# Optimization experiments

Hardware: AMD Instinct MI355X
Metric: run time of the kernel (lower is better)

Reference implementation:

```python
import jax, jax.numpy as jnp
import numpy as np

N = 50000          # nodes
E = 800000         # edges (avg degree 16)
NODE_IN, NODE_OUT = 64, 96
EDGE_IN, EDGE_OUT = 32, 32
CONV = [192, 192]  # hidden_conv_sizes
LIN = [192]        # hidden_linear_sizes
NUM_CLASSES = 2


def _linear_init(k, fan_in, fan_out):
    s = 1.0 / np.sqrt(fan_in)
    kw, kb = jax.random.split(k)
    W = jax.random.uniform(kw, (fan_in, fan_out), jnp.float32, -s, s)
    b = jax.random.uniform(kb, (fan_out,), jnp.float32, -s, s)
    return W, b


def setup_inputs() -> dict:
    key = jax.random.key(0)
    ks = jax.random.split(key, 10)
    node_feats = jax.random.normal(ks[0], (N, NODE_IN), jnp.float32)
    edge_feats = jax.random.normal(ks[1], (E, EDGE_IN), jnp.float32)
    src = jax.random.randint(ks[2], (E,), 0, N)
    dst = jax.random.randint(ks[3], (E,), 0, N)
    Wn, bn = _linear_init(ks[4], NODE_IN, NODE_OUT)
    We, be = _linear_init(ks[5], EDGE_IN, EDGE_OUT)
    Wc0, bc0 = _linear_init(ks[6], NODE_OUT + EDGE_OUT, CONV[0])
    Wc1, bc1 = _linear_init(ks[7], CONV[0], CONV[1])
    Wl0, bl0 = _linear_init(ks[8], CONV[1], LIN[0])
    Wo, bo = _linear_init(ks[9], LIN[0], NUM_CLASSES)
    return dict(node_feats=node_feats, edge_feats=edge_feats,
                Wn=Wn, bn=bn, We=We, be=be,
                Wc0=Wc0, bc0=bc0, Wc1=Wc1, bc1=bc1,
                Wl0=Wl0, bl0=bl0, Wo=Wo, bo=bo,
                src=src, dst=dst)


def reference(node_feats, edge_feats, Wn, bn, We, be, Wc0, bc0, Wc1, bc1,
              Wl0, bl0, Wo, bo, src, dst):
    ones = jnp.ones((E,), jnp.float32)
    deg_in = jnp.clip(jax.ops.segment_sum(ones, dst, num_segments=N), 1.0)
    deg_out = jnp.clip(jax.ops.segment_sum(ones, src, num_segments=N), 1.0)
    inv_in = jax.lax.rsqrt(deg_in)    # D_in^{-1/2}
    inv_out = jax.lax.rsqrt(deg_out)  # D_out^{-1/2}

    # EdgeLayer: per-edge linear, mean-aggregated onto destination nodes
    eh = edge_feats @ We + be                                   # [E, EDGE_OUT]
    edge_h = jax.nn.relu(
        jax.ops.segment_sum(eh, dst, num_segments=N) / deg_in[:, None])

    # NodeEmbeddingLayer: per-node linear
    node_h = jax.nn.relu(node_feats @ Wn + bn)                  # [N, NODE_OUT]

    h = jnp.concatenate([edge_h, node_h], axis=1)               # [N, EDGE_OUT+NODE_OUT]

    # dgl GraphConv (norm='both'): D_in^{-1/2} A D_out^{-1/2} h W + b
    # dropout is identity in eval mode
    for W, b in ((Wc0, bc0), (Wc1, bc1)):
        msg = (h * inv_out[:, None])[src]                       # [E, d] gather
        agg = jax.ops.segment_sum(msg, dst, num_segments=N) * inv_in[:, None]
        h = jax.nn.relu(agg @ W + b)

    h = jax.nn.relu(h @ Wl0 + bl0)
    return h @ Wo + bo                                          # [N, NUM_CLASSES]
```

## Files before the change

kernel.cpp:

```cpp
#include <hip/hip_runtime.h>

#define NN 50000
#define NE 800000
#define CAP 64

#define NPB 128
#define NBKT 391
#define NBKT_PAD 512
#define BCAP 3072
#define CHUNK 4096

typedef unsigned short u16;
typedef unsigned int u32;
typedef unsigned long long u64;
typedef __attribute__((ext_vector_type(8))) short bf8_t;
typedef __attribute__((ext_vector_type(4))) float f4_t;

__device__ __forceinline__ u16 f2b(float f) {
    unsigned u = __float_as_uint(f);
    unsigned r = u + 0x7FFF + ((u >> 16) & 1);
    return (u16)(r >> 16);
}

__global__ __launch_bounds__(256) void partition_k(
    const int* __restrict__ src, const int* __restrict__ dst,
    int* __restrict__ deg_out, int* __restrict__ bktc,
    u64* __restrict__ part, int E) {
    __shared__ unsigned cnt[NBKT_PAD];
    __shared__ unsigned base[NBKT_PAD];
    __shared__ unsigned cur[NBKT_PAD];
    __shared__ unsigned gbase[NBKT_PAD];
    __shared__ unsigned wtot[4];
    __shared__ u64 staged[CHUNK];

    const int tid = threadIdx.x;
    const int lane = tid & 63;
    const int wid = tid >> 6;
    const int e0 = blockIdx.x * CHUNK;
    const int n = min(CHUNK, E - e0);

    for (int i = tid; i < NBKT_PAD; i += 256) cnt[i] = 0;
    __syncthreads();

    for (int i = tid; i < n; i += 256) {
        int d = dst[e0 + i];
        atomicAdd(&cnt[d >> 7], 1u);
    }
    __syncthreads();

    {
        unsigned a = cnt[2 * tid];
        unsigned b = cnt[2 * tid + 1];
        unsigned ps = a + b;
        unsigned inc = ps;
#pragma unroll
        for (int d = 1; d < 64; d <<= 1) {
            unsigned v = __shfl_up(inc, d);
            if (lane >= d) inc += v;
        }
        if (lane == 63) wtot[wid] = inc;
        __syncthreads();
        unsigned wb = 0;
#pragma unroll
        for (int k = 0; k < 4; ++k) wb += (k < wid) ? wtot[k] : 0;
        unsigned eb = wb + inc - ps;
        base[2 * tid] = eb;
        base[2 * tid + 1] = eb + a;
        cur[2 * tid] = eb;
        cur[2 * tid + 1] = eb + a;
    }
    __syncthreads();

    for (int i = tid; i < n; i += 256) {
        int e = e0 + i;
        int d = dst[e];
        int s = src[e];
        atomicAdd(deg_out + s, 1);
        unsigned p = atomicAdd(&cur[d >> 7], 1u);
        staged[p] = ((u64)(unsigned)e << 32) | (((u32)d << 16) | (u32)s);
    }
    __syncthreads();

    for (int b = tid; b < NBKT; b += 256) {
        unsigned c = cur[b] - base[b];
        if (c) gbase[b] = (unsigned)atomicAdd(&bktc[b], (int)c);
    }
    __syncthreads();

    for (int i = tid; i < n; i += 256) {
        u64 v = staged[i];
        int b = (int)((v >> 16) & 0xffffu) >> 7;
        unsigned idx = gbase[b] + ((unsigned)i - base[b]);
        if (idx < BCAP) part[(size_t)b * BCAP + idx] = v;
    }
}

__global__ __launch_bounds__(256) void fill_k(
    const u64* __restrict__ part, const int* __restrict__ bktc,
    int* __restrict__ csr_src, int* __restrict__ csr_eid,
    int* __restrict__ din, int n) {
    __shared__ unsigned cur[NPB];
    const int tid = threadIdx.x;
    const int b = blockIdx.x;
    const int node0 = b << 7;
    if (tid < NPB) cur[tid] = 0;
    __syncthreads();

    const int cnt = min(bktc[b], BCAP);
    const u64* p = part + (size_t)b * BCAP;
    for (int i = tid; i < cnt; i += 256) {
        u64 v = p[i];
        int s = (int)(v & 0xffffu);
        int d = (int)((v >> 16) & 0xffffu);
        int e = (int)(v >> 32);
        unsigned q = atomicAdd(&cur[d & (NPB - 1)], 1u);
        if (q < CAP) {
            csr_src[((size_t)d << 6) + q] = s;
            csr_eid[((size_t)d << 6) + q] = e;
        }
    }
    __syncthreads();
    if (tid < NPB) {
        int node = node0 + tid;
        if (node < n) {
            unsigned cq = min(cur[tid], (unsigned)CAP);
            din[node] = (int)cq;
            int end = (cq <= 32u) ? 32 : 64;
            for (int q = (int)cq; q < end; ++q)
                csr_eid[((size_t)node << 6) + q] = 0;
        }
    }
}

__global__ void make_inv_k(const int* __restrict__ deg_in, const int* __restrict__ deg_out,
                           float* __restrict__ inv_in, float* __restrict__ inv_out,
                           float* __restrict__ inv_mean, float* __restrict__ bcoef, int n) {
    int i = blockIdx.x * 256 + threadIdx.x;
    if (i < n) {
        int d_in = deg_in[i];
        float di = fmaxf((float)d_in, 1.0f);
        float dq = fmaxf((float)deg_out[i], 1.0f);
        inv_in[i]   = 1.0f / sqrtf(di);
        inv_out[i]  = 1.0f / sqrtf(dq);
        inv_mean[i] = 1.0f / di;
        bcoef[i]    = (d_in > 0) ? 1.0f : 0.0f;
    }
}

__global__ __launch_bounds__(256) void gather_e4_k(
    const float* __restrict__ ef, const int* __restrict__ csr_eid,
    const int* __restrict__ deg, float* __restrict__ efa) {
    const int lane = threadIdx.x & 63;
    const int node = __builtin_amdgcn_readfirstlane(blockIdx.x * 4 + (threadIdx.x >> 6));
    const int beg = node << 6;
    const int cnt = deg[node];
    const int g = lane >> 4;
    const int c = (lane & 15) * 2;

    float ax = 0.0f, ay = 0.0f;
    {
        int eidv[8];
#pragma unroll
        for (int j = 0; j < 8; ++j) eidv[j] = csr_eid[beg + 4 * j + g];
        float2 v[8];
#pragma unroll
        for (int j = 0; j < 8; ++j)
            v[j] = *(const float2*)(ef + (size_t)eidv[j] * 32 + c);
#pragma unroll
        for (int j = 0; j < 8; ++j)
            if (4 * j + g < cnt) { ax += v[j].x; ay += v[j].y; }
    }
    if (cnt > 32) {
        int eidv[8];
#pragma unroll
        for (int j = 0; j < 8; ++j) eidv[j] = csr_eid[beg + 32 + 4 * j + g];
        float2 v[8];
#pragma unroll
        for (int j = 0; j < 8; ++j)
            v[j] = *(const float2*)(ef + (size_t)eidv[j] * 32 + c);
#pragma unroll
        for (int j = 0; j < 8; ++j)
            if (32 + 4 * j + g < cnt) { ax += v[j].x; ay += v[j].y; }
    }
    ax += __shfl_down(ax, 16); ay += __shfl_down(ay, 16);
    ax += __shfl_down(ax, 32); ay += __shfl_down(ay, 32);
    if (lane < 16) {
        float2 o; o.x = ax; o.y = ay;
        *(float2*)(efa + (size_t)node * 32 + c) = o;
    }
}

template <int D, int LPT>
__global__ __launch_bounds__(256) void gather_b2_k(
    const u16* __restrict__ h, const int* __restrict__ csr,
    const int* __restrict__ deg, const float* __restrict__ inv_in,
    u16* __restrict__ agg) {
    constexpr int ACT = D / LPT;
    constexpr int NW = LPT / 2;
    const int lane = threadIdx.x & 63;
    const int node = __builtin_amdgcn_readfirstlane(blockIdx.x * 4 + (threadIdx.x >> 6));
    const int beg = node << 6;
    const int cnt = deg[node];
    const int off = (lane < ACT ? lane : ACT - 1) * LPT;

    float acc[LPT];
#pragma unroll
    for (int j = 0; j < LPT; ++j) acc[j] = 0.0f;

    const int nb = cnt >> 4;
    int idx[16];
    if (nb > 0) {
#pragma unroll
        for (int j = 0; j < 16; ++j) idx[j] = csr[beg + j];
    }
    for (int b = 0; b < nb; ++b) {
        unsigned lv[16][NW];
#pragma unroll
        for (int j = 0; j < 16; ++j) {
            const unsigned* p = (const unsigned*)(h + (size_t)idx[j] * D + off);
            if constexpr (NW == 2) {
                uint2 t = *(const uint2*)p;
                lv[j][0] = t.x; lv[j][1] = t.y;
            } else {
                lv[j][0] = *p;
            }
        }
        int nidx[16];
        const int nbase = beg + (b + 1) * 16;
        if (b + 1 < nb) {
#pragma unroll
            for (int j = 0; j < 16; ++j) nidx[j] = csr[nbase + j];
        }
#pragma unroll
        for (int j = 0; j < 16; ++j)
#pragma unroll
            for (int q = 0; q < NW; ++q) {
                unsigned u = lv[j][q];
                acc[2 * q]     += __uint_as_float(u << 16);
                acc[2 * q + 1] += __uint_as_float(u & 0xffff0000u);
            }
        if (b + 1 < nb) {
#pragma unroll
            for (int j = 0; j < 16; ++j) idx[j] = nidx[j];
        }
    }

    int tb = beg + (nb << 4);
    int rem = cnt & 15;
    if (rem >= 8) {
        int ti[8];
#pragma unroll
        for (int j = 0; j < 8; ++j) ti[j] = csr[tb + j];
        unsigned lv[8][NW];
#pragma unroll
        for (int j = 0; j < 8; ++j) {
            const unsigned* p = (const unsigned*)(h + (size_t)ti[j] * D + off);
            if constexpr (NW == 2) {
                uint2 t = *(const uint2*)p;
                lv[j][0] = t.x; lv[j][1] = t.y;
            } else {
                lv[j][0] = *p;
            }
        }
#pragma unroll
        for (int j = 0; j < 8; ++j)
#pragma unroll
            for (int q = 0; q < NW; ++q) {
                unsigned u = lv[j][q];
                acc[2 * q]     += __uint_as_float(u << 16);
                acc[2 * q + 1] += __uint_as_float(u & 0xffff0000u);
            }
        tb += 8;
        rem -= 8;
    }
    for (int t = 0; t < rem; ++t) {
        const unsigned* p = (const unsigned*)(h + (size_t)csr[tb + t] * D + off);
#pragma unroll
        for (int q = 0; q < NW; ++q) {
            unsigned u = p[q];
            acc[2 * q]     += __uint_as_float(u << 16);
            acc[2 * q + 1] += __uint_as_float(u & 0xffff0000u);
        }
    }

    if (lane < ACT) {
        float sc = inv_in[node];
        unsigned o[NW];
#pragma unroll
        for (int q = 0; q < NW; ++q)
            o[q] = (unsigned)f2b(acc[2 * q] * sc) | ((unsigned)f2b(acc[2 * q + 1] * sc) << 16);
        unsigned* dp = (unsigned*)(agg + (size_t)node * D + off);
        if constexpr (NW == 2) {
            uint2 t; t.x = o[0]; t.y = o[1];
            *(uint2*)dp = t;
        } else {
            *dp = o[0];
        }
    }
}

template <int D_IN, int D_OUT, bool SCALE, bool BROW>
__global__ __launch_bounds__(256) void gemm_tile_k(
    const float* __restrict__ in, int in_stride,
    const float* __restrict__ W, const float* __restrict__ bias,
    const float* __restrict__ scale, const float* __restrict__ brow,
    const float* __restrict__ posts,
    u16* __restrict__ out, int out_stride, int n) {
    constexpr int TMW = 8;
    constexpr int ROWS = TMW * 4;
    constexpr int NOUT = (D_OUT + 63) / 64;
    __shared__ float s_in[ROWS * D_IN];

    const int tid = threadIdx.x;
    const int lane = tid & 63;
    const int wave = tid >> 6;
    const int row0 = blockIdx.x * ROWS;

    constexpr int NV = ROWS * D_IN / 4;
    for (int i = tid; i < NV; i += 256) {
        int m = i / (D_IN / 4);
        int kv = i % (D_IN / 4);
        int row = min(row0 + m, n - 1);
        float4 v = *(const float4*)(in + (size_t)row * in_stride + kv * 4);
        if (SCALE) {
            float s = scale[row];
            v.x *= s; v.y *= s; v.z *= s; v.w *= s;
        }
        *(float4*)(s_in + m * D_IN + kv * 4) = v;
    }
    __syncthreads();

    int f[NOUT], ff[NOUT];
    bool fok[NOUT];
    float bv[NOUT];
#pragma unroll
    for (int o = 0; o < NOUT; ++o) {
        f[o] = lane + 64 * o;
        fok[o] = (f[o] < D_OUT);
        ff[o] = fok[o] ? f[o] : 0;
        bv[o] = bias[ff[o]];
    }

    const float* s_my = s_in + wave * TMW * D_IN;

    float acc[NOUT][TMW];
#pragma unroll
    for (int o = 0; o < NOUT; ++o)
#pragma unroll
        for (int m = 0; m < TMW; ++m) acc[o][m] = 0.0f;

    for (int k = 0; k < D_IN; k += 4) {
        float w[4][NOUT];
#pragma unroll
        for (int j = 0; j < 4; ++j)
#pragma unroll
            for (int o = 0; o < NOUT; ++o) w[j][o] = W[(k + j) * D_OUT + ff[o]];
#pragma unroll
        for (int m = 0; m < TMW; ++m) {
            float4 a = *(const float4*)(s_my + m * D_IN + k);
#pragma unroll
            for (int o = 0; o < NOUT; ++o) {
                acc[o][m] = fmaf(a.x, w[0][o], acc[o][m]);
                acc[o][m] = fmaf(a.y, w[1][o], acc[o][m]);
                acc[o][m] = fmaf(a.z, w[2][o], acc[o][m]);
                acc[o][m] = fmaf(a.w, w[3][o], acc[o][m]);
            }
        }
    }

#pragma unroll
    for (int m = 0; m < TMW; ++m) {
        int row = row0 + wave * TMW + m;
        if (row < n) {
            float bc = BROW ? brow[row] : 1.0f;
            float pm = posts[row];
#pragma unroll
            for (int o = 0; o < NOUT; ++o) {
                if (!fok[o]) continue;
                float v = fmaxf(acc[o][m] + bv[o] * bc, 0.0f) * pm;
                out[(size_t)row * out_stride + f[o]] = f2b(v);
            }
        }
    }
}

template <int K>
__global__ void pack_w_k(const float* __restrict__ W, u16* __restrict__ Wp) {
    constexpr int KS = K / 32;
    int idx = blockIdx.x * 256 + threadIdx.x;
    if (idx >= 12 * KS * 64) return;
    int l = idx & 63;
    int s = (idx >> 6) % KS;
    int t = (idx >> 6) / KS;
    int col = t * 16 + (l & 15);
    int krow = s * 32 + ((l >> 4) * 8);
    u16 tmp[8] __attribute__((aligned(16)));
#pragma unroll
    for (int j = 0; j < 8; ++j) tmp[j] = f2b(W[(size_t)(krow + j) * 192 + col]);
    *(uint4*)(Wp + (size_t)idx * 8) = *(const uint4*)tmp;
}

template <int K>
__global__ __launch_bounds__(256) void mfma_gemm_k(
    const u16* __restrict__ A, const u16* __restrict__ Wp,
    const float* __restrict__ bias, const float* __restrict__ posts,
    u16* __restrict__ outB, int n) {
    constexpr int KS = K / 32;
    const int tid = threadIdx.x;
    const int lane = tid & 63;
    const int w = tid >> 6;
    const int row0 = blockIdx.x * 16;
    const int arow = row0 + (lane & 15);
    const int kbase = (lane >> 4) * 8;

    f4_t acc[3];
#pragma unroll
    for (int o = 0; o < 3; ++o) acc[o] = (f4_t){0.f, 0.f, 0.f, 0.f};

    const u16* ap = A + (size_t)arow * K + kbase;
#pragma unroll
    for (int s = 0; s < KS; ++s) {
        bf8_t af = *(const bf8_t*)(ap + s * 32);
#pragma unroll
        for (int o = 0; o < 3; ++o) {
            int t = w * 3 + o;
            bf8_t bf = *(const bf8_t*)(Wp + (size_t)((t * KS + s) * 64 + lane) * 8);
            acc[o] = __builtin_amdgcn_mfma_f32_16x16x32_bf16(af, bf, acc[o], 0, 0, 0);
        }
    }

    const int drow = row0 + (lane >> 4) * 4;
    const int dcol = lane & 15;
    float pm[4];
#pragma unroll
    for (int r = 0; r < 4; ++r) pm[r] = posts[drow + r];
#pragma unroll
    for (int o = 0; o < 3; ++o) {
        int col = (w * 3 + o) * 16 + dcol;
        float bv = bias[col];
#pragma unroll
        for (int r = 0; r < 4; ++r) {
            float v = fmaxf(acc[o][r] + bv, 0.0f) * pm[r];
            outB[(size_t)(drow + r) * 192 + col] = f2b(v);
        }
    }
}

__global__ __launch_bounds__(256) void mfma_fused_k(
    const u16* __restrict__ A,
    const u16* __restrict__ Wp1, const float* __restrict__ b1,
    const u16* __restrict__ Wp2, const float* __restrict__ b2,
    const float* __restrict__ Wo, const float* __restrict__ bo,
    float* __restrict__ out, int n) {
    constexpr int KS = 6;
    constexpr int S = 200;
    __shared__ float sbuf[16 * S];
    __shared__ float s_head[16][17][2];

    const int tid = threadIdx.x;
    const int lane = tid & 63;
    const int w = tid >> 6;
    const int row0 = blockIdx.x * 16;
    const int arow = row0 + (lane & 15);
    const int kbase = (lane >> 4) * 8;
    const int drow = (lane >> 4) * 4;
    const int dcol = lane & 15;

    f4_t acc[3];
#pragma unroll
    for (int o = 0; o < 3; ++o) acc[o] = (f4_t){0.f, 0.f, 0.f, 0.f};

    const u16* ap = A + (size_t)arow * 192 + kbase;
#pragma unroll
    for (int s = 0; s < KS; ++s) {
        bf8_t af = *(const bf8_t*)(ap + s * 32);
#pragma unroll
        for (int o = 0; o < 3; ++o) {
            int t = w * 3 + o;
            bf8_t bf = *(const bf8_t*)(Wp1 + (size_t)((t * KS + s) * 64 + lane) * 8);
            acc[o] = __builtin_amdgcn_mfma_f32_16x16x32_bf16(af, bf, acc[o], 0, 0, 0);
        }
    }

    u16* h2 = (u16*)sbuf;
#pragma unroll
    for (int o = 0; o < 3; ++o) {
        int col = (w * 3 + o) * 16 + dcol;
        float bv = b1[col];
#pragma unroll
        for (int r = 0; r < 4; ++r)
            h2[(drow + r) * S + col] = f2b(fmaxf(acc[o][r] + bv, 0.0f));
    }
    __syncthreads();

#pragma unroll
    for (int o = 0; o < 3; ++o) acc[o] = (f4_t){0.f, 0.f, 0.f, 0.f};
    const u16* hp = h2 + (lane & 15) * S + kbase;
#pragma unroll
    for (int s = 0; s < KS; ++s) {
        bf8_t af = *(const bf8_t*)(hp + s * 32);
#pragma unroll
        for (int o = 0; o < 3; ++o) {
            int t = w * 3 + o;
            bf8_t bf = *(const bf8_t*)(Wp2 + (size_t)((t * KS + s) * 64 + lane) * 8);
            acc[o] = __builtin_amdgcn_mfma_f32_16x16x32_bf16(af, bf, acc[o], 0, 0, 0);
        }
    }
    __syncthreads();

#pragma unroll
    for (int o = 0; o < 3; ++o) {
        int col = (w * 3 + o) * 16 + dcol;
        float bv = b2[col];
#pragma unroll
        for (int r = 0; r < 4; ++r)
            sbuf[(drow + r) * S + col] = fmaxf(acc[o][r] + bv, 0.0f);
    }
    __syncthreads();

    {
        int r = tid >> 4;
        int seg = tid & 15;
        const float* hr = sbuf + r * S + seg * 12;
        const float* wor = Wo + seg * 24;
        float p0 = 0.0f, p1 = 0.0f;
#pragma unroll
        for (int c = 0; c < 12; ++c) {
            float hv = hr[c];
            p0 = fmaf(hv, wor[c * 2 + 0], p0);
            p1 = fmaf(hv, wor[c * 2 + 1], p1);
        }
        s_head[r][seg][0] = p0;
        s_head[r][seg][1] = p1;
    }
    __syncthreads();
    if (tid < 32) {
        int r = tid >> 1, c = tid & 1;
        float sum = bo[c];
#pragma unroll
        for (int g = 0; g < 16; ++g) sum += s_head[r][g][c];
        int row = row0 + r;
        if (row < n) out[(size_t)row * 2 + c] = sum;
    }
}

extern "C" void kernel_launch(void* const* d_in, const int* in_sizes, int n_in,
                              void* d_out, int out_size, void* d_ws, size_t ws_size,
                              hipStream_t stream) {
    const float* node_feats = (const float*)d_in[0];
    const float* edge_feats = (const float*)d_in[1];
    const float* Wn  = (const float*)d_in[2];
    const float* bn  = (const float*)d_in[3];
    const float* We  = (const float*)d_in[4];
    const float* be  = (const float*)d_in[5];
    const float* Wc0 = (const float*)d_in[6];
    const float* bc0 = (const float*)d_in[7];
    const float* Wc1 = (const float*)d_in[8];
    const float* bc1 = (const float*)d_in[9];
    const float* Wl0 = (const float*)d_in[10];
    const float* bl0 = (const float*)d_in[11];
    const float* Wo  = (const float*)d_in[12];
    const float* bo  = (const float*)d_in[13];
    const int* src = (const int*)d_in[14];
    const int* dst = (const int*)d_in[15];
    float* out = (float*)d_out;

    const int N = NN, E = NE;

    int* dout      = (int*)d_ws;
    int* bktc      = dout + N;
    int* din       = bktc + NBKT_PAD;
    int* csr_src   = din + N;
    int* csr_eid   = csr_src + (size_t)CAP * N;
    float* inv_in   = (float*)(csr_eid + (size_t)CAP * N);
    float* inv_out  = inv_in + N;
    float* inv_mean = inv_out + N;
    float* bcoef    = inv_mean + N;
    float* efa      = bcoef + N;
    u16* h0   = (u16*)(efa + (size_t)32 * N);
    u16* aggA = h0 + (size_t)128 * N;
    u16* h1   = aggA + (size_t)128 * N;
    u16* aggB = h1 + (size_t)192 * N;
    u16* Wp0  = aggB + (size_t)192 * N;
    u16* Wp1  = Wp0 + 128 * 192;
    u16* Wp2  = Wp1 + 192 * 192;
    u64* part = (u64*)h1;

    hipMemsetAsync(d_ws, 0, (size_t)(N + NBKT_PAD) * sizeof(int), stream);

    const int GB32 = (N + 31) / 32;
    const int GB16 = N / 16;
    const int GW4  = (N + 3) / 4;

    pack_w_k<128><<<dim3(12), dim3(256), 0, stream>>>(Wc0, Wp0);
    pack_w_k<192><<<dim3(18), dim3(256), 0, stream>>>(Wc1, Wp1);
    pack_w_k<192><<<dim3(18), dim3(256), 0, stream>>>(Wl0, Wp2);

    partition_k<<<dim3((E + CHUNK - 1) / CHUNK), dim3(256), 0, stream>>>(
        src, dst, dout, bktc, part, E);
    fill_k<<<dim3(NBKT), dim3(256), 0, stream>>>(part, bktc, csr_src, csr_eid, din, N);
    make_inv_k<<<dim3((N + 255) / 256), dim3(256), 0, stream>>>(din, dout, inv_in, inv_out,
                                                                inv_mean, bcoef, N);

    gather_e4_k<<<dim3(GW4), dim3(256), 0, stream>>>(edge_feats, csr_eid, din, efa);

    gemm_tile_k<32, 32, true, true><<<dim3(GB32), dim3(256), 0, stream>>>(
        efa, 32, We, be, inv_mean, bcoef, inv_out, h0, 128, N);
    gemm_tile_k<64, 96, false, false><<<dim3(GB32), dim3(256), 0, stream>>>(
        node_feats, 64, Wn, bn, nullptr, nullptr, inv_out, h0 + 32, 128, N);

    gather_b2_k<128, 2><<<dim3(GW4), dim3(256), 0, stream>>>(h0, csr_src, din, inv_in, aggA);
    mfma_gemm_k<128><<<dim3(GB16), dim3(256), 0, stream>>>(aggA, Wp0, bc0, inv_out, h1, N);

    gather_b2_k<192, 4><<<dim3(GW4), dim3(256), 0, stream>>>(h1, csr_src, din, inv_in, aggB);
    mfma_fused_k<<<dim3(GB16), dim3(256), 0, stream>>>(aggB, Wp1, bc1, Wp2, bl0, Wo, bo,
                                                       out, N);
}
```

Measured before the change: 429.6 us.

## Apply edge linear per-edge via MFMA before gathering, fold inv into fill

Instead of gathering the fp32 edge features (128 B per edge) and then applying the edge linear per node, the edge linear is applied to every edge with a bf16 MFMA kernel. The result goes to a bf16 edge buffer (64 B per edge), and the gather then reads half the bytes and writes straight into h0 with mean, bias, ReLU and the inv_out scale applied. The make_inv kernel is merged into fill_k, which removes a launch. The trade-offs are an extra full pass writing 800k×32 bf16 values and lower precision from rounding the edge features and outputs to bf16.

```diff
diff --git a/kernel.cpp b/kernel.cpp
--- a/kernel.cpp
+++ b/kernel.cpp
@@ -97,8 +97,11 @@
 
 __global__ __launch_bounds__(256) void fill_k(
     const u64* __restrict__ part, const int* __restrict__ bktc,
+    const int* __restrict__ deg_out,
     int* __restrict__ csr_src, int* __restrict__ csr_eid,
-    int* __restrict__ din, int n) {
+    int* __restrict__ din,
+    float* __restrict__ inv_in, float* __restrict__ inv_out,
+    float* __restrict__ inv_mean, float* __restrict__ bcoef, int n) {
     __shared__ unsigned cur[NPB];
     const int tid = threadIdx.x;
     const int b = blockIdx.x;
@@ -128,65 +131,121 @@
             int end = (cq <= 32u) ? 32 : 64;
             for (int q = (int)cq; q < end; ++q)
                 csr_eid[((size_t)node << 6) + q] = 0;
-        }
-    }
-}
-
-__global__ void make_inv_k(const int* __restrict__ deg_in, const int* __restrict__ deg_out,
-                           float* __restrict__ inv_in, float* __restrict__ inv_out,
-                           float* __restrict__ inv_mean, float* __restrict__ bcoef, int n) {
-    int i = blockIdx.x * 256 + threadIdx.x;
-    if (i < n) {
-        int d_in = deg_in[i];
-        float di = fmaxf((float)d_in, 1.0f);
-        float dq = fmaxf((float)deg_out[i], 1.0f);
-        inv_in[i]   = 1.0f / sqrtf(di);
-        inv_out[i]  = 1.0f / sqrtf(dq);
-        inv_mean[i] = 1.0f / di;
-        bcoef[i]    = (d_in > 0) ? 1.0f : 0.0f;
-    }
-}
-
-__global__ __launch_bounds__(256) void gather_e4_k(
-    const float* __restrict__ ef, const int* __restrict__ csr_eid,
-    const int* __restrict__ deg, float* __restrict__ efa) {
+            float di = fmaxf((float)cq, 1.0f);
+            float dq = fmaxf((float)deg_out[node], 1.0f);
+            inv_in[node]   = 1.0f / sqrtf(di);
+            inv_out[node]  = 1.0f / sqrtf(dq);
+            inv_mean[node] = 1.0f / di;
+            bcoef[node]    = (cq > 0u) ? 1.0f : 0.0f;
+        }
+    }
+}
+
+__global__ void pack_we_k(const float* __restrict__ We, u16* __restrict__ WpE) {
+    int idx = threadIdx.x;
+    if (idx >= 128) return;
+    int l = idx & 63;
+    int t = idx >> 6;
+    int col = t * 16 + (l & 15);
+    int krow = (l >> 4) * 8;
+    u16 tmp[8] __attribute__((aligned(16)));
+#pragma unroll
+    for (int j = 0; j < 8; ++j) tmp[j] = f2b(We[(size_t)(krow + j) * 32 + col]);
+    *(uint4*)(WpE + (size_t)idx * 8) = *(const uint4*)tmp;
+}
+
+__global__ __launch_bounds__(256) void edge_mlp_k(
+    const float* __restrict__ ef, const u16* __restrict__ WpE,
+    u16* __restrict__ eh, int E) {
+    __shared__ u16 sout[4][16 * 32];
+    const int tid = threadIdx.x;
+    const int lane = tid & 63;
+    const int w = tid >> 6;
+    const int row0 = (blockIdx.x * 4 + w) * 16;
+    const int arow = row0 + (lane & 15);
+    const int kbase = (lane >> 4) * 8;
+
+    const float* ap = ef + (size_t)arow * 32 + kbase;
+    float4 a0 = *(const float4*)(ap);
+    float4 a1 = *(const float4*)(ap + 4);
+    u16 av[8] __attribute__((aligned(16)));
+    av[0] = f2b(a0.x); av[1] = f2b(a0.y); av[2] = f2b(a0.z); av[3] = f2b(a0.w);
+    av[4] = f2b(a1.x); av[5] = f2b(a1.y); av[6] = f2b(a1.z); av[7] = f2b(a1.w);
+    bf8_t af = *(const bf8_t*)av;
+
+    f4_t acc[2];
+#pragma unroll
+    for (int o = 0; o < 2; ++o) {
+        bf8_t bf = *(const bf8_t*)(WpE + (size_t)(o * 64 + lane) * 8);
+        acc[o] = __builtin_amdgcn_mfma_f32_16x16x32_bf16(af, bf, (f4_t){0.f,0.f,0.f,0.f},
+                                                         0, 0, 0);
+    }
+
+    const int drow = (lane >> 4) * 4;
+    const int dcol = lane & 15;
+#pragma unroll
+    for (int o = 0; o < 2; ++o)
+#pragma unroll
+        for (int r = 0; r < 4; ++r)
+            sout[w][(drow + r) * 32 + o * 16 + dcol] = f2b(acc[o][r]);
+    uint4 v = *(const uint4*)&sout[w][lane * 8];
+    *(uint4*)(eh + (size_t)row0 * 32 + lane * 8) = v;
+}
+
+__global__ __launch_bounds__(256) void gather_eh_k(
+    const u16* __restrict__ eh, const int* __restrict__ csr_eid,
+    const int* __restrict__ deg,
+    const float* __restrict__ inv_mean, const float* __restrict__ bcoef,
+    const float* __restrict__ inv_out, const float* __restrict__ be,
+    u16* __restrict__ h0) {
     const int lane = threadIdx.x & 63;
     const int node = __builtin_amdgcn_readfirstlane(blockIdx.x * 4 + (threadIdx.x >> 6));
     const int beg = node << 6;
     const int cnt = deg[node];
     const int g = lane >> 4;
-    const int c = (lane & 15) * 2;
+    const int c = lane & 15;
 
     float ax = 0.0f, ay = 0.0f;
     {
         int eidv[8];
 #pragma unroll
         for (int j = 0; j < 8; ++j) eidv[j] = csr_eid[beg + 4 * j + g];
-        float2 v[8];
+        unsigned uv[8];
 #pragma unroll
         for (int j = 0; j < 8; ++j)
-            v[j] = *(const float2*)(ef + (size_t)eidv[j] * 32 + c);
+            uv[j] = *(const unsigned*)(eh + (size_t)eidv[j] * 32 + 2 * c);
 #pragma unroll
         for (int j = 0; j < 8; ++j)
-            if (4 * j + g < cnt) { ax += v[j].x; ay += v[j].y; }
+            if (4 * j + g < cnt) {
+                ax += __uint_as_float(uv[j] << 16);
+                ay += __uint_as_float(uv[j] & 0xffff0000u);
+            }
     }
     if (cnt > 32) {
         int eidv[8];
 #pragma unroll
         for (int j = 0; j < 8; ++j) eidv[j] = csr_eid[beg + 32 + 4 * j + g];
-        float2 v[8];
+        unsigned uv[8];
 #pragma unroll
         for (int j = 0; j < 8; ++j)
-            v[j] = *(const float2*)(ef + (size_t)eidv[j] * 32 + c);
+            uv[j] = *(const unsigned*)(eh + (size_t)eidv[j] * 32 + 2 * c);
 #pragma unroll
         for (int j = 0; j < 8; ++j)
-            if (32 + 4 * j + g < cnt) { ax += v[j].x; ay += v[j].y; }
+            if (32 + 4 * j + g < cnt) {
+                ax += __uint_as_float(uv[j] << 16);
+                ay += __uint_as_float(uv[j] & 0xffff0000u);
+            }
     }
     ax += __shfl_down(ax, 16); ay += __shfl_down(ay, 16);
     ax += __shfl_down(ax, 32); ay += __shfl_down(ay, 32);
     if (lane < 16) {
-        float2 o; o.x = ax; o.y = ay;
-        *(float2*)(efa + (size_t)node * 32 + c) = o;
+        float im = inv_mean[node];
+        float bc = bcoef[node];
+        float po = inv_out[node];
+        float v0 = fmaxf(ax * im + be[2 * c] * bc, 0.0f) * po;
+        float v1 = fmaxf(ay * im + be[2 * c + 1] * bc, 0.0f) * po;
+        unsigned o = (unsigned)f2b(v0) | ((unsigned)f2b(v1) << 16);
+        *(unsigned*)(h0 + (size_t)node * 128 + 2 * c) = o;
     }
 }
 
@@ -576,14 +635,15 @@
     float* inv_out  = inv_in + N;
     float* inv_mean = inv_out + N;
     float* bcoef    = inv_mean + N;
-    float* efa      = bcoef + N;
-    u16* h0   = (u16*)(efa + (size_t)32 * N);
+    u16* h0   = (u16*)(bcoef + N);
     u16* aggA = h0 + (size_t)128 * N;
     u16* h1   = aggA + (size_t)128 * N;
     u16* aggB = h1 + (size_t)192 * N;
     u16* Wp0  = aggB + (size_t)192 * N;
     u16* Wp1  = Wp0 + 128 * 192;
     u16* Wp2  = Wp1 + 192 * 192;
+    u16* WpE  = Wp2 + 192 * 192;
+    u16* eh   = WpE + 1024;
     u64* part = (u64*)h1;
 
     hipMemsetAsync(d_ws, 0, (size_t)(N + NBKT_PAD) * sizeof(int), stream);
@@ -591,21 +651,21 @@
     const int GB32 = (N + 31) / 32;
     const int GB16 = N / 16;
     const int GW4  = (N + 3) / 4;
+    const int GEM  = E / 64;
 
     pack_w_k<128><<<dim3(12), dim3(256), 0, stream>>>(Wc0, Wp0);
     pack_w_k<192><<<dim3(18), dim3(256), 0, stream>>>(Wc1, Wp1);
     pack_w_k<192><<<dim3(18), dim3(256), 0, stream>>>(Wl0, Wp2);
+    pack_we_k<<<dim3(1), dim3(128), 0, stream>>>(We, WpE);
 
     partition_k<<<dim3((E + CHUNK - 1) / CHUNK), dim3(256), 0, stream>>>(
         src, dst, dout, bktc, part, E);
-    fill_k<<<dim3(NBKT), dim3(256), 0, stream>>>(part, bktc, csr_src, csr_eid, din, N);
-    make_inv_k<<<dim3((N + 255) / 256), dim3(256), 0, stream>>>(din, dout, inv_in, inv_out,
-                                                                inv_mean, bcoef, N);
-
-    gather_e4_k<<<dim3(GW4), dim3(256), 0, stream>>>(edge_feats, csr_eid, din, efa);
-
-    gemm_tile_k<32, 32, true, true><<<dim3(GB32), dim3(256), 0, stream>>>(
-        efa, 32, We, be, inv_mean, bcoef, inv_out, h0, 128, N);
+    fill_k<<<dim3(NBKT), dim3(256), 0, stream>>>(part, bktc, dout, csr_src, csr_eid,
+                                                 din, inv_in, inv_out, inv_mean, bcoef, N);
+
+    edge_mlp_k<<<dim3(GEM), dim3(256), 0, stream>>>(edge_feats, WpE, eh, E);
+    gather_eh_k<<<dim3(GW4), dim3(256), 0, stream>>>(eh, csr_eid, din, inv_mean, bcoef,
+                                                     inv_out, be, h0);
     gemm_tile_k<64, 96, false, false><<<dim3(GB32), dim3(256), 0, stream>>>(
         node_feats, 64, Wn, bn, nullptr, nullptr, inv_out, h0 + 32, 128, N);
 
```

Result: no change. 428.7 us (-0.2%).

## Fuse neighbor gathers into conv GEMMs and edge aggregation into edge MLP

Applied to the files above, without the earlier changes.

Each graph-conv gather now writes its aggregated rows into a shared-memory tile, and the MFMA GEMM runs from that tile in the same kernel. This removes the aggA/aggB global intermediates and their extra kernel launches. The edge-feature mean aggregation is fused with the 32x32 edge linear layer, so efa disappears. The inverse-degree computation moves into fill_k, and the three weight-pack kernels are merged into one. The trade-off is less memory-level parallelism in the gathers: each wave now processes four nodes one after another inside a 16-row block, which may hide gather latency less well.

```diff
diff --git a/kernel.cpp b/kernel.cpp
--- a/kernel.cpp
+++ b/kernel.cpp
@@ -97,8 +97,11 @@
 
 __global__ __launch_bounds__(256) void fill_k(
     const u64* __restrict__ part, const int* __restrict__ bktc,
+    const int* __restrict__ deg_out,
     int* __restrict__ csr_src, int* __restrict__ csr_eid,
-    int* __restrict__ din, int n) {
+    int* __restrict__ din,
+    float* __restrict__ inv_in, float* __restrict__ inv_out,
+    float* __restrict__ inv_mean, float* __restrict__ bcoef, int n) {
     __shared__ unsigned cur[NPB];
     const int tid = threadIdx.x;
     const int b = blockIdx.x;
@@ -128,34 +131,55 @@
             int end = (cq <= 32u) ? 32 : 64;
             for (int q = (int)cq; q < end; ++q)
                 csr_eid[((size_t)node << 6) + q] = 0;
-        }
-    }
-}
-
-__global__ void make_inv_k(const int* __restrict__ deg_in, const int* __restrict__ deg_out,
-                           float* __restrict__ inv_in, float* __restrict__ inv_out,
-                           float* __restrict__ inv_mean, float* __restrict__ bcoef, int n) {
-    int i = blockIdx.x * 256 + threadIdx.x;
-    if (i < n) {
-        int d_in = deg_in[i];
-        float di = fmaxf((float)d_in, 1.0f);
-        float dq = fmaxf((float)deg_out[i], 1.0f);
-        inv_in[i]   = 1.0f / sqrtf(di);
-        inv_out[i]  = 1.0f / sqrtf(dq);
-        inv_mean[i] = 1.0f / di;
-        bcoef[i]    = (d_in > 0) ? 1.0f : 0.0f;
-    }
-}
-
-__global__ __launch_bounds__(256) void gather_e4_k(
+            float di = fmaxf((float)cq, 1.0f);
+            float dq = fmaxf((float)deg_out[node], 1.0f);
+            inv_in[node]   = 1.0f / sqrtf(di);
+            inv_out[node]  = 1.0f / sqrtf(dq);
+            inv_mean[node] = 1.0f / di;
+            bcoef[node]    = (cq > 0u) ? 1.0f : 0.0f;
+        }
+    }
+}
+
+__device__ __forceinline__ void pack_one(const float* __restrict__ W, u16* __restrict__ Wp,
+                                         int idx, int KS) {
+    int l = idx & 63;
+    int s = (idx >> 6) % KS;
+    int t = (idx >> 6) / KS;
+    int col = t * 16 + (l & 15);
+    int krow = s * 32 + ((l >> 4) * 8);
+    u16 tmp[8] __attribute__((aligned(16)));
+#pragma unroll
+    for (int j = 0; j < 8; ++j) tmp[j] = f2b(W[(size_t)(krow + j) * 192 + col]);
+    *(uint4*)(Wp + (size_t)idx * 8) = *(const uint4*)tmp;
+}
+
+__global__ void pack_all_k(const float* __restrict__ Wc0, const float* __restrict__ Wc1,
+                           const float* __restrict__ Wl0,
+                           u16* __restrict__ Wp0, u16* __restrict__ Wp1,
+                           u16* __restrict__ Wp2) {
+    int idx = blockIdx.x * 256 + threadIdx.x;
+    if (idx < 3072) pack_one(Wc0, Wp0, idx, 4);
+    else if (idx < 7680) pack_one(Wc1, Wp1, idx - 3072, 6);
+    else if (idx < 12288) pack_one(Wl0, Wp2, idx - 7680, 6);
+}
+
+__global__ __launch_bounds__(256) void edge_gather_mlp_k(
     const float* __restrict__ ef, const int* __restrict__ csr_eid,
-    const int* __restrict__ deg, float* __restrict__ efa) {
-    const int lane = threadIdx.x & 63;
-    const int node = __builtin_amdgcn_readfirstlane(blockIdx.x * 4 + (threadIdx.x >> 6));
+    const int* __restrict__ deg,
+    const float* __restrict__ inv_mean, const float* __restrict__ bcoef,
+    const float* __restrict__ inv_out,
+    const float* __restrict__ We, const float* __restrict__ be,
+    u16* __restrict__ h0) {
+    __shared__ float sv[4][32];
+    const int tid = threadIdx.x;
+    const int lane = tid & 63;
+    const int w = tid >> 6;
+    const int node = __builtin_amdgcn_readfirstlane(blockIdx.x * 4 + w);
     const int beg = node << 6;
     const int cnt = deg[node];
     const int g = lane >> 4;
-    const int c = (lane & 15) * 2;
+    const int c = lane & 15;
 
     float ax = 0.0f, ay = 0.0f;
     {
@@ -165,7 +189,7 @@
         float2 v[8];
 #pragma unroll
         for (int j = 0; j < 8; ++j)
-            v[j] = *(const float2*)(ef + (size_t)eidv[j] * 32 + c);
+            v[j] = *(const float2*)(ef + (size_t)eidv[j] * 32 + 2 * c);
 #pragma unroll
         for (int j = 0; j < 8; ++j)
             if (4 * j + g < cnt) { ax += v[j].x; ay += v[j].y; }
@@ -177,7 +201,7 @@
         float2 v[8];
 #pragma unroll
         for (int j = 0; j < 8; ++j)
-            v[j] = *(const float2*)(ef + (size_t)eidv[j] * 32 + c);
+            v[j] = *(const float2*)(ef + (size_t)eidv[j] * 32 + 2 * c);
 #pragma unroll
         for (int j = 0; j < 8; ++j)
             if (32 + 4 * j + g < cnt) { ax += v[j].x; ay += v[j].y; }
@@ -185,28 +209,25 @@
     ax += __shfl_down(ax, 16); ay += __shfl_down(ay, 16);
     ax += __shfl_down(ax, 32); ay += __shfl_down(ay, 32);
     if (lane < 16) {
-        float2 o; o.x = ax; o.y = ay;
-        *(float2*)(efa + (size_t)node * 32 + c) = o;
-    }
-}
-
-template <int D, int LPT>
-__global__ __launch_bounds__(256) void gather_b2_k(
+        float im = inv_mean[node];
+        float2 o; o.x = ax * im; o.y = ay * im;
+        *(float2*)&sv[w][2 * c] = o;
+    }
+    int col = lane & 31;
+    float s = 0.0f;
+#pragma unroll 8
+    for (int k = 0; k < 32; ++k)
+        s = fmaf(sv[w][k], We[k * 32 + col], s);
+    if (lane < 32) {
+        float v = fmaxf(s + be[col] * bcoef[node], 0.0f) * inv_out[node];
+        h0[(size_t)node * 128 + col] = f2b(v);
+    }
+}
+
+__device__ __forceinline__ void gather_node_d128(
     const u16* __restrict__ h, const int* __restrict__ csr,
-    const int* __restrict__ deg, const float* __restrict__ inv_in,
-    u16* __restrict__ agg) {
-    constexpr int ACT = D / LPT;
-    constexpr int NW = LPT / 2;
-    const int lane = threadIdx.x & 63;
-    const int node = __builtin_amdgcn_readfirstlane(blockIdx.x * 4 + (threadIdx.x >> 6));
-    const int beg = node << 6;
-    const int cnt = deg[node];
-    const int off = (lane < ACT ? lane : ACT - 1) * LPT;
-
-    float acc[LPT];
-#pragma unroll
-    for (int j = 0; j < LPT; ++j) acc[j] = 0.0f;
-
+    int beg, int cnt, int off, float& a0, float& a1) {
+    a0 = 0.0f; a1 = 0.0f;
     const int nb = cnt >> 4;
     int idx[16];
     if (nb > 0) {
@@ -214,17 +235,10 @@
         for (int j = 0; j < 16; ++j) idx[j] = csr[beg + j];
     }
     for (int b = 0; b < nb; ++b) {
-        unsigned lv[16][NW];
-#pragma unroll
-        for (int j = 0; j < 16; ++j) {
-            const unsigned* p = (const unsigned*)(h + (size_t)idx[j] * D + off);
-            if constexpr (NW == 2) {
-                uint2 t = *(const uint2*)p;
-                lv[j][0] = t.x; lv[j][1] = t.y;
-            } else {
-                lv[j][0] = *p;
-            }
-        }
+        unsigned lv[16];
+#pragma unroll
+        for (int j = 0; j < 16; ++j)
+            lv[j] = *(const unsigned*)(h + (size_t)idx[j] * 128 + off);
         int nidx[16];
         const int nbase = beg + (b + 1) * 16;
         if (b + 1 < nb) {
@@ -232,9 +246,67 @@
             for (int j = 0; j < 16; ++j) nidx[j] = csr[nbase + j];
         }
 #pragma unroll
+        for (int j = 0; j < 16; ++j) {
+            a0 += __uint_as_float(lv[j] << 16);
+            a1 += __uint_as_float(lv[j] & 0xffff0000u);
+        }
+        if (b + 1 < nb) {
+#pragma unroll
+            for (int j = 0; j < 16; ++j) idx[j] = nidx[j];
+        }
+    }
+    int tb = beg + (nb << 4);
+    int rem = cnt & 15;
+    if (rem >= 8) {
+        int ti[8];
+#pragma unroll
+        for (int j = 0; j < 8; ++j) ti[j] = csr[tb + j];
+        unsigned lv[8];
+#pragma unroll
+        for (int j = 0; j < 8; ++j)
+            lv[j] = *(const unsigned*)(h + (size_t)ti[j] * 128 + off);
+#pragma unroll
+        for (int j = 0; j < 8; ++j) {
+            a0 += __uint_as_float(lv[j] << 16);
+            a1 += __uint_as_float(lv[j] & 0xffff0000u);
+        }
+        tb += 8; rem -= 8;
+    }
+    for (int t = 0; t < rem; ++t) {
+        unsigned u = *(const unsigned*)(h + (size_t)csr[tb + t] * 128 + off);
+        a0 += __uint_as_float(u << 16);
+        a1 += __uint_as_float(u & 0xffff0000u);
+    }
+}
+
+__device__ __forceinline__ void gather_node_d192(
+    const u16* __restrict__ h, const int* __restrict__ csr,
+    int beg, int cnt, int off, float* acc) {
+#pragma unroll
+    for (int j = 0; j < 4; ++j) acc[j] = 0.0f;
+    const int nb = cnt >> 4;
+    int idx[16];
+    if (nb > 0) {
+#pragma unroll
+        for (int j = 0; j < 16; ++j) idx[j] = csr[beg + j];
+    }
+    for (int b = 0; b < nb; ++b) {
+        unsigned lv[16][2];
+#pragma unroll
+        for (int j = 0; j < 16; ++j) {
+            uint2 t = *(const uint2*)(h + (size_t)idx[j] * 192 + off);
+            lv[j][0] = t.x; lv[j][1] = t.y;
+        }
+        int nidx[16];
+        const int nbase = beg + (b + 1) * 16;
+        if (b + 1 < nb) {
+#pragma unroll
+            for (int j = 0; j < 16; ++j) nidx[j] = csr[nbase + j];
+        }
+#pragma unroll
         for (int j = 0; j < 16; ++j)
 #pragma unroll
-            for (int q = 0; q < NW; ++q) {
+            for (int q = 0; q < 2; ++q) {
                 unsigned u = lv[j][q];
                 acc[2 * q]     += __uint_as_float(u << 16);
                 acc[2 * q + 1] += __uint_as_float(u & 0xffff0000u);
@@ -244,66 +316,212 @@
             for (int j = 0; j < 16; ++j) idx[j] = nidx[j];
         }
     }
-
     int tb = beg + (nb << 4);
     int rem = cnt & 15;
     if (rem >= 8) {
         int ti[8];
 #pragma unroll
         for (int j = 0; j < 8; ++j) ti[j] = csr[tb + j];
-        unsigned lv[8][NW];
+        unsigned lv[8][2];
 #pragma unroll
         for (int j = 0; j < 8; ++j) {
-            const unsigned* p = (const unsigned*)(h + (size_t)ti[j] * D + off);
-            if constexpr (NW == 2) {
-                uint2 t = *(const uint2*)p;
-                lv[j][0] = t.x; lv[j][1] = t.y;
-            } else {
-                lv[j][0] = *p;
-            }
+            uint2 t = *(const uint2*)(h + (size_t)ti[j] * 192 + off);
+            lv[j][0] = t.x; lv[j][1] = t.y;
         }
 #pragma unroll
         for (int j = 0; j < 8; ++j)
 #pragma unroll
-            for (int q = 0; q < NW; ++q) {
+            for (int q = 0; q < 2; ++q) {
                 unsigned u = lv[j][q];
                 acc[2 * q]     += __uint_as_float(u << 16);
                 acc[2 * q + 1] += __uint_as_float(u & 0xffff0000u);
             }
-        tb += 8;
-        rem -= 8;
+        tb += 8; rem -= 8;
     }
     for (int t = 0; t < rem; ++t) {
-        const unsigned* p = (const unsigned*)(h + (size_t)csr[tb + t] * D + off);
-#pragma unroll
-        for (int q = 0; q < NW; ++q) {
+        const unsigned* p = (const unsigned*)(h + (size_t)csr[tb + t] * 192 + off);
+#pragma unroll
+        for (int q = 0; q < 2; ++q) {
             unsigned u = p[q];
             acc[2 * q]     += __uint_as_float(u << 16);
             acc[2 * q + 1] += __uint_as_float(u & 0xffff0000u);
         }
     }
-
-    if (lane < ACT) {
+}
+
+__global__ __launch_bounds__(256) void conv0_k(
+    const u16* __restrict__ h0, const int* __restrict__ csr,
+    const int* __restrict__ deg, const float* __restrict__ inv_in,
+    const u16* __restrict__ Wp, const float* __restrict__ bias,
+    const float* __restrict__ posts, u16* __restrict__ h1) {
+    constexpr int KS = 4, ST = 136;
+    __shared__ u16 tile[16 * ST];
+    const int tid = threadIdx.x;
+    const int lane = tid & 63;
+    const int w = tid >> 6;
+    const int row0 = blockIdx.x * 16;
+    const int off = lane * 2;
+
+    for (int t = 0; t < 4; ++t) {
+        const int node = row0 + w * 4 + t;
+        float a0, a1;
+        gather_node_d128(h0, csr, node << 6, deg[node], off, a0, a1);
         float sc = inv_in[node];
-        unsigned o[NW];
-#pragma unroll
-        for (int q = 0; q < NW; ++q)
-            o[q] = (unsigned)f2b(acc[2 * q] * sc) | ((unsigned)f2b(acc[2 * q + 1] * sc) << 16);
-        unsigned* dp = (unsigned*)(agg + (size_t)node * D + off);
-        if constexpr (NW == 2) {
-            uint2 t; t.x = o[0]; t.y = o[1];
-            *(uint2*)dp = t;
-        } else {
-            *dp = o[0];
-        }
-    }
-}
-
-template <int D_IN, int D_OUT, bool SCALE, bool BROW>
+        unsigned o = (unsigned)f2b(a0 * sc) | ((unsigned)f2b(a1 * sc) << 16);
+        *(unsigned*)&tile[(w * 4 + t) * ST + off] = o;
+    }
+    __syncthreads();
+
+    const int kbase = (lane >> 4) * 8;
+    f4_t acc[3];
+#pragma unroll
+    for (int o = 0; o < 3; ++o) acc[o] = (f4_t){0.f, 0.f, 0.f, 0.f};
+    const u16* ap = tile + (lane & 15) * ST + kbase;
+#pragma unroll
+    for (int s = 0; s < KS; ++s) {
+        bf8_t af = *(const bf8_t*)(ap + s * 32);
+#pragma unroll
+        for (int o = 0; o < 3; ++o) {
+            int t = w * 3 + o;
+            bf8_t bf = *(const bf8_t*)(Wp + (size_t)((t * KS + s) * 64 + lane) * 8);
+            acc[o] = __builtin_amdgcn_mfma_f32_16x16x32_bf16(af, bf, acc[o], 0, 0, 0);
+        }
+    }
+
+    const int drow = row0 + (lane >> 4) * 4;
+    const int dcol = lane & 15;
+    float pm[4];
+#pragma unroll
+    for (int r = 0; r < 4; ++r) pm[r] = posts[drow + r];
+#pragma unroll
+    for (int o = 0; o < 3; ++o) {
+        int col = (w * 3 + o) * 16 + dcol;
+        float bv = bias[col];
+#pragma unroll
+        for (int r = 0; r < 4; ++r) {
+            float v = fmaxf(acc[o][r] + bv, 0.0f) * pm[r];
+            h1[(size_t)(drow + r) * 192 + col] = f2b(v);
+        }
+    }
+}
+
+__global__ __launch_bounds__(256) void conv1_k(
+    const u16* __restrict__ h1, const int* __restrict__ csr,
+    const int* __restrict__ deg, const float* __restrict__ inv_in,
+    const u16* __restrict__ Wp1, const float* __restrict__ b1,
+    const u16* __restrict__ Wp2, const float* __restrict__ b2,
+    const float* __restrict__ Wo, const float* __restrict__ bo,
+    float* __restrict__ out, int n) {
+    constexpr int KS = 6, S = 200;
+    __shared__ u16 tileA[16 * S];
+    __shared__ float sbuf[16 * S];
+    __shared__ float s_head[16][17][2];
+
+    const int tid = threadIdx.x;
+    const int lane = tid & 63;
+    const int w = tid >> 6;
+    const int row0 = blockIdx.x * 16;
+    const int kbase = (lane >> 4) * 8;
+    const int drow = (lane >> 4) * 4;
+    const int dcol = lane & 15;
+    const int goff = (lane < 48 ? lane : 47) * 4;
+
+    for (int t = 0; t < 4; ++t) {
+        const int node = row0 + w * 4 + t;
+        float acc4[4];
+        gather_node_d192(h1, csr, node << 6, deg[node], goff, acc4);
+        if (lane < 48) {
+            float sc = inv_in[node];
+            uint2 o;
+            o.x = (unsigned)f2b(acc4[0] * sc) | ((unsigned)f2b(acc4[1] * sc) << 16);
+            o.y = (unsigned)f2b(acc4[2] * sc) | ((unsigned)f2b(acc4[3] * sc) << 16);
+            *(uint2*)&tileA[(w * 4 + t) * S + goff] = o;
+        }
+    }
+    __syncthreads();
+
+    f4_t acc[3];
+#pragma unroll
+    for (int o = 0; o < 3; ++o) acc[o] = (f4_t){0.f, 0.f, 0.f, 0.f};
+
+    const u16* ap = tileA + (lane & 15) * S + kbase;
+#pragma unroll
+    for (int s = 0; s < KS; ++s) {
+        bf8_t af = *(const bf8_t*)(ap + s * 32);
+#pragma unroll
+        for (int o = 0; o < 3; ++o) {
+            int t = w * 3 + o;
+            bf8_t bf = *(const bf8_t*)(Wp1 + (size_t)((t * KS + s) * 64 + lane) * 8);
+            acc[o] = __builtin_amdgcn_mfma_f32_16x16x32_bf16(af, bf, acc[o], 0, 0, 0);
+        }
+    }
+
+    u16* h2 = (u16*)sbuf;
+#pragma unroll
+    for (int o = 0; o < 3; ++o) {
+        int col = (w * 3 + o) * 16 + dcol;
+        float bv = b1[col];
+#pragma unroll
+        for (int r = 0; r < 4; ++r)
+            h2[(drow + r) * S + col] = f2b(fmaxf(acc[o][r] + bv, 0.0f));
+    }
+    __syncthreads();
+
+#pragma unroll
+    for (int o = 0; o < 3; ++o) acc[o] = (f4_t){0.f, 0.f, 0.f, 0.f};
+    const u16* hp = h2 + (lane & 15) * S + kbase;
+#pragma unroll
+    for (int s = 0; s < KS; ++s) {
+        bf8_t af = *(const bf8_t*)(hp + s * 32);
+#pragma unroll
+        for (int o = 0; o < 3; ++o) {
+            int t = w * 3 + o;
+            bf8_t bf = *(const bf8_t*)(Wp2 + (size_t)((t * KS + s) * 64 + lane) * 8);
+            acc[o] = __builtin_amdgcn_mfma_f32_16x16x32_bf16(af, bf, acc[o], 0, 0, 0);
+        }
+    }
+    __syncthreads();
+
+#pragma unroll
+    for (int o = 0; o < 3; ++o) {
+        int col = (w * 3 + o) * 16 + dcol;
+        float bv = b2[col];
+#pragma unroll
+        for (int r = 0; r < 4; ++r)
+            sbuf[(drow + r) * S + col] = fmaxf(acc[o][r] + bv, 0.0f);
+    }
+    __syncthreads();
+
+    {
+        int r = tid >> 4;
+        int seg = tid & 15;
+        const float* hr = sbuf + r * S + seg * 12;
+        const float* wor = Wo + seg * 24;
+        float p0 = 0.0f, p1 = 0.0f;
+#pragma unroll
+        for (int c = 0; c < 12; ++c) {
+            float hv = hr[c];
+            p0 = fmaf(hv, wor[c * 2 + 0], p0);
+            p1 = fmaf(hv, wor[c * 2 + 1], p1);
+        }
+        s_head[r][seg][0] = p0;
+        s_head[r][seg][1] = p1;
+    }
+    __syncthreads();
+    if (tid < 32) {
+        int r = tid >> 1, c = tid & 1;
+        float sum = bo[c];
+#pragma unroll
+        for (int g = 0; g < 16; ++g) sum += s_head[r][g][c];
+        int row = row0 + r;
+        if (row < n) out[(size_t)row * 2 + c] = sum;
+    }
+}
+
+template <int D_IN, int D_OUT>
 __global__ __launch_bounds__(256) void gemm_tile_k(
     const float* __restrict__ in, int in_stride,
     const float* __restrict__ W, const float* __restrict__ bias,
-    const float* __restrict__ scale, const float* __restrict__ brow,
     const float* __restrict__ posts,
     u16* __restrict__ out, int out_stride, int n) {
     constexpr int TMW = 8;
@@ -322,10 +540,6 @@
         int kv = i % (D_IN / 4);
         int row = min(row0 + m, n - 1);
         float4 v = *(const float4*)(in + (size_t)row * in_stride + kv * 4);
-        if (SCALE) {
-            float s = scale[row];
-            v.x *= s; v.y *= s; v.z *= s; v.w *= s;
-        }
         *(float4*)(s_in + m * D_IN + kv * 4) = v;
     }
     __syncthreads();
@@ -372,175 +586,14 @@
     for (int m = 0; m < TMW; ++m) {
         int row = row0 + wave * TMW + m;
         if (row < n) {
-            float bc = BROW ? brow[row] : 1.0f;
             float pm = posts[row];
 #pragma unroll
             for (int o = 0; o < NOUT; ++o) {
                 if (!fok[o]) continue;
-                float v = fmaxf(acc[o][m] + bv[o] * bc, 0.0f) * pm;
+                float v = fmaxf(acc[o][m] + bv[o], 0.0f) * pm;
                 out[(size_t)row * out_stride + f[o]] = f2b(v);
             }
         }
-    }
-}
-
-template <int K>
-__global__ void pack_w_k(const float* __restrict__ W, u16* __restrict__ Wp) {
-    constexpr int KS = K / 32;
-    int idx = blockIdx.x * 256 + threadIdx.x;
-    if (idx >= 12 * KS * 64) return;
-    int l = idx & 63;
-    int s = (idx >> 6) % KS;
-    int t = (idx >> 6) / KS;
-    int col = t * 16 + (l & 15);
-    int krow = s * 32 + ((l >> 4) * 8);
-    u16 tmp[8] __attribute__((aligned(16)));
-#pragma unroll
-    for (int j = 0; j < 8; ++j) tmp[j] = f2b(W[(size_t)(krow + j) * 192 + col]);
-    *(uint4*)(Wp + (size_t)idx * 8) = *(const uint4*)tmp;
-}
-
-template <int K>
-__global__ __launch_bounds__(256) void mfma_gemm_k(
-    const u16* __restrict__ A, const u16* __restrict__ Wp,
-    const float* __restrict__ bias, const float* __restrict__ posts,
-    u16* __restrict__ outB, int n) {
-    constexpr int KS = K / 32;
-    const int tid = threadIdx.x;
-    const int lane = tid & 63;
-    const int w = tid >> 6;
-    const int row0 = blockIdx.x * 16;
-    const int arow = row0 + (lane & 15);
-    const int kbase = (lane >> 4) * 8;
-
-    f4_t acc[3];
-#pragma unroll
-    for (int o = 0; o < 3; ++o) acc[o] = (f4_t){0.f, 0.f, 0.f, 0.f};
-
-    const u16* ap = A + (size_t)arow * K + kbase;
-#pragma unroll
-    for (int s = 0; s < KS; ++s) {
-        bf8_t af = *(const bf8_t*)(ap + s * 32);
-#pragma unroll
-        for (int o = 0; o < 3; ++o) {
-            int t = w * 3 + o;
-            bf8_t bf = *(const bf8_t*)(Wp + (size_t)((t * KS + s) * 64 + lane) * 8);
-            acc[o] = __builtin_amdgcn_mfma_f32_16x16x32_bf16(af, bf, acc[o], 0, 0, 0);
-        }
-    }
-
-    const int drow = row0 + (lane >> 4) * 4;
-    const int dcol = lane & 15;
-    float pm[4];
-#pragma unroll
-    for (int r = 0; r < 4; ++r) pm[r] = posts[drow + r];
-#pragma unroll
-    for (int o = 0; o < 3; ++o) {
-        int col = (w * 3 + o) * 16 + dcol;
-        float bv = bias[col];
-#pragma unroll
-        for (int r = 0; r < 4; ++r) {
-            float v = fmaxf(acc[o][r] + bv, 0.0f) * pm[r];
-            outB[(size_t)(drow + r) * 192 + col] = f2b(v);
-        }
-    }
-}
-
-__global__ __launch_bounds__(256) void mfma_fused_k(
-    const u16* __restrict__ A,
-    const u16* __restrict__ Wp1, const float* __restrict__ b1,
-    const u16* __restrict__ Wp2, const float* __restrict__ b2,
-    const float* __restrict__ Wo, const float* __restrict__ bo,
-    float* __restrict__ out, int n) {
-    constexpr int KS = 6;
-    constexpr int S = 200;
-    __shared__ float sbuf[16 * S];
-    __shared__ float s_head[16][17][2];
-
-    const int tid = threadIdx.x;
-    const int lane = tid & 63;
-    const int w = tid >> 6;
-    const int row0 = blockIdx.x * 16;
-    const int arow = row0 + (lane & 15);
-    const int kbase = (lane >> 4) * 8;
-    const int drow = (lane >> 4) * 4;
-    const int dcol = lane & 15;
-
-    f4_t acc[3];
-#pragma unroll
-    for (int o = 0; o < 3; ++o) acc[o] = (f4_t){0.f, 0.f, 0.f, 0.f};
-
-    const u16* ap = A + (size_t)arow * 192 + kbase;
-#pragma unroll
-    for (int s = 0; s < KS; ++s) {
-        bf8_t af = *(const bf8_t*)(ap + s * 32);
-#pragma unroll
-        for (int o = 0; o < 3; ++o) {
-            int t = w * 3 + o;
-            bf8_t bf = *(const bf8_t*)(Wp1 + (size_t)((t * KS + s) * 64 + lane) * 8);
-            acc[o] = __builtin_amdgcn_mfma_f32_16x16x32_bf16(af, bf, acc[o], 0, 0, 0);
-        }
-    }
-
-    u16* h2 = (u16*)sbuf;
-#pragma unroll
-    for (int o = 0; o < 3; ++o) {
-        int col = (w * 3 + o) * 16 + dcol;
-        float bv = b1[col];
-#pragma unroll
-        for (int r = 0; r < 4; ++r)
-            h2[(drow + r) * S + col] = f2b(fmaxf(acc[o][r] + bv, 0.0f));
-    }
-    __syncthreads();
-
-#pragma unroll
-    for (int o = 0; o < 3; ++o) acc[o] = (f4_t){0.f, 0.f, 0.f, 0.f};
-    const u16* hp = h2 + (lane & 15) * S + kbase;
-#pragma unroll
-    for (int s = 0; s < KS; ++s) {
-        bf8_t af = *(const bf8_t*)(hp + s * 32);
-#pragma unroll
-        for (int o = 0; o < 3; ++o) {
-            int t = w * 3 + o;
-            bf8_t bf = *(const bf8_t*)(Wp2 + (size_t)((t * KS + s) * 64 + lane) * 8);
-            acc[o] = __builtin_amdgcn_mfma_f32_16x16x32_bf16(af, bf, acc[o], 0, 0, 0);
-        }
-    }
-    __syncthreads();
-
-#pragma unroll
-    for (int o = 0; o < 3; ++o) {
-        int col = (w * 3 + o) * 16 + dcol;
-        float bv = b2[col];
-#pragma unroll
-        for (int r = 0; r < 4; ++r)
-            sbuf[(drow + r) * S + col] = fmaxf(acc[o][r] + bv, 0.0f);
-    }
-    __syncthreads();
-
-    {
-        int r = tid >> 4;
-        int seg = tid & 15;
-        const float* hr = sbuf + r * S + seg * 12;
-        const float* wor = Wo + seg * 24;
-        float p0 = 0.0f, p1 = 0.0f;
-#pragma unroll
-        for (int c = 0; c < 12; ++c) {
-            float hv = hr[c];
-            p0 = fmaf(hv, wor[c * 2 + 0], p0);
-            p1 = fmaf(hv, wor[c * 2 + 1], p1);
-        }
-        s_head[r][seg][0] = p0;
-        s_head[r][seg][1] = p1;
-    }
-    __syncthreads();
-    if (tid < 32) {
-        int r = tid >> 1, c = tid & 1;
-        float sum = bo[c];
-#pragma unroll
-        for (int g = 0; g < 16; ++g) sum += s_head[r][g][c];
-        int row = row0 + r;
-        if (row < n) out[(size_t)row * 2 + c] = sum;
     }
 }
 
@@ -576,12 +629,9 @@
     float* inv_out  = inv_in + N;
     float* inv_mean = inv_out + N;
     float* bcoef    = inv_mean + N;
-    float* efa      = bcoef + N;
-    u16* h0   = (u16*)(efa + (size_t)32 * N);
-    u16* aggA = h0 + (size_t)128 * N;
-    u16* h1   = aggA + (size_t)128 * N;
-    u16* aggB = h1 + (size_t)192 * N;
-    u16* Wp0  = aggB + (size_t)192 * N;
+    u16* h0   = (u16*)(bcoef + N);
+    u16* h1   = h0 + (size_t)128 * N;
+    u16* Wp0  = h1 + (size_t)192 * N;
     u16* Wp1  = Wp0 + 128 * 192;
     u16* Wp2  = Wp1 + 192 * 192;
     u64* part = (u64*)h1;
@@ -592,27 +642,20 @@
     const int GB16 = N / 16;
     const int GW4  = (N + 3) / 4;
 
-    pack_w_k<128><<<dim3(12), dim3(256), 0, stream>>>(Wc0, Wp0);
-    pack_w_k<192><<<dim3(18), dim3(256), 0, stream>>>(Wc1, Wp1);
-    pack_w_k<192><<<dim3(18), dim3(256), 0, stream>>>(Wl0, Wp2);
+    pack_all_k<<<dim3(48), dim3(256), 0, stream>>>(Wc0, Wc1, Wl0, Wp0, Wp1, Wp2);
 
     partition_k<<<dim3((E + CHUNK - 1) / CHUNK), dim3(256), 0, stream>>>(
         src, dst, dout, bktc, part, E);
-    fill_k<<<dim3(NBKT), dim3(256), 0, stream>>>(part, bktc, csr_src, csr_eid, din, N);
-    make_inv_k<<<dim3((N + 255) / 256), dim3(256), 0, stream>>>(din, dout, inv_in, inv_out,
-                                                                inv_mean, bcoef, N);
-
-    gather_e4_k<<<dim3(GW4), dim3(256), 0, stream>>>(edge_feats, csr_eid, din, efa);
-
-    gemm_tile_k<32, 32, true, true><<<dim3(GB32), dim3(256), 0, stream>>>(
-        efa, 32, We, be, inv_mean, bcoef, inv_out, h0, 128, N);
-    gemm_tile_k<64, 96, false, false><<<dim3(GB32), dim3(256), 0, stream>>>(
-        node_feats, 64, Wn, bn, nullptr, nullptr, inv_out, h0 + 32, 128, N);
-
-    gather_b2_k<128, 2><<<dim3(GW4), dim3(256), 0, stream>>>(h0, csr_src, din, inv_in, aggA);
-    mfma_gemm_k<128><<<dim3(GB16), dim3(256), 0, stream>>>(aggA, Wp0, bc0, inv_out, h1, N);
-
-    gather_b2_k<192, 4><<<dim3(GW4), dim3(256), 0, stream>>>(h1, csr_src, din, inv_in, aggB);
-    mfma_fused_k<<<dim3(GB16), dim3(256), 0, stream>>>(aggB, Wp1, bc1, Wp2, bl0, Wo, bo,
-                                                       out, N);
-}
+    fill_k<<<dim3(NBKT), dim3(256), 0, stream>>>(part, bktc, dout, csr_src, csr_eid,
+                                                 din, inv_in, inv_out, inv_mean, bcoef, N);
+
+    edge_gather_mlp_k<<<dim3(GW4), dim3(256), 0, stream>>>(
+        edge_feats, csr_eid, din, inv_mean, bcoef, inv_out, We, be, h0);
+    gemm_tile_k<64, 96><<<dim3(GB32), dim3(256), 0, stream>>>(
+        node_feats, 64, Wn, bn, inv_out, h0 + 32, 128, N);
+
+    conv0_k<<<dim3(GB16), dim3(256), 0, stream>>>(h0, csr_src, din, inv_in,
+                                                  Wp0, bc0, inv_out, h1);
+    conv1_k<<<dim3(GB16), dim3(256), 0, stream>>>(h1, csr_src, din, inv_in,
+                                                  Wp1, bc1, Wp2, bl0, Wo, bo, out, N);
+}
```

Measured after the change: 451.5 us. +5.1%, slower.
